# Kernel optimization log

Measured on AMD Instinct MI355X. Metric: run time of the kernel, lower is better.

## Reference

```python
import jax, jax.numpy as jnp
import numpy as np

N_NODES = 50000
BN_EPS = 1e-5


def setup_inputs() -> dict:
    key = jax.random.key(0)
    ks = jax.random.split(key, 10)
    n, e, d, L = N_NODES, 500000, 128, 2
    x = jax.random.normal(ks[0], (n, d), dtype=jnp.float32)
    edge_index = jax.random.randint(ks[1], (2, e), 0, n, dtype=jnp.int64)
    edge_attr = jax.random.normal(ks[2], (e, d), dtype=jnp.float32)
    W1 = jax.random.normal(ks[3], (L, d, d), dtype=jnp.float32) * 0.05
    b1 = jax.random.normal(ks[4], (L, d), dtype=jnp.float32) * 0.02
    gamma = 1.0 + 0.1 * jax.random.normal(ks[5], (L, d), dtype=jnp.float32)
    beta = 0.1 * jax.random.normal(ks[6], (L, d), dtype=jnp.float32)
    W2 = jax.random.normal(ks[7], (L, d, d), dtype=jnp.float32) * 0.05
    b2 = jax.random.normal(ks[8], (L, d), dtype=jnp.float32) * 0.02
    return {"x": x, "edge_index": edge_index, "edge_attr": edge_attr,
            "W1": W1, "b1": b1, "gamma": gamma, "beta": beta, "W2": W2, "b2": b2}


def _gine_layer(x, src, dst, edge_attr, W1l, b1l, gl, bl, W2l, b2l):
    # GINEConv message: relu(x_j + edge_attr), sum-aggregated to target nodes
    msg = jax.nn.relu(x[src] + edge_attr)              # [E, d]
    agg = jax.ops.segment_sum(msg, dst, num_segments=N_NODES)  # [N, d]
    h = (x + agg) @ W1l + b1l                           # eps=0 -> (1+eps)*x = x
    # BatchNorm1d over nodes (train-mode batch stats, biased var)
    mu = jnp.mean(h, axis=0)
    var = jnp.mean(jnp.square(h - mu), axis=0)
    h = (h - mu) * jax.lax.rsqrt(var + BN_EPS) * gl + bl
    h = jax.nn.relu(h)
    h = jax.nn.relu(h @ W2l + b2l)
    return jax.nn.relu(h)  # encoder's outer activation


def reference(x, edge_index, edge_attr, W1, b1, gamma, beta, W2, b2):
    src, dst = edge_index[0], edge_index[1]
    L = W1.shape[0]
    for l in range(L):
        x = _gine_layer(x, src, dst, edge_attr, W1[l], b1[l], gamma[l], beta[l], W2[l], b2[l])
    return x
```

## Files before the change

### kernel.cpp

```cpp
#include <hip/hip_runtime.h>

#define BN_EPS 1e-5f

using f4 = __attribute__((ext_vector_type(4))) float;
using h4 = __attribute__((ext_vector_type(4))) _Float16;

__device__ inline f4 relu4(f4 v) {
    v.x = fmaxf(v.x, 0.f); v.y = fmaxf(v.y, 0.f);
    v.z = fmaxf(v.z, 0.f); v.w = fmaxf(v.w, 0.f);
    return v;
}

__global__ __launch_bounds__(256) void detect_i64_kernel(const int* __restrict__ ei,
                                                         int* __restrict__ flag, int npairs,
                                                         int* __restrict__ deg, int N) {
    __shared__ int ok;
    if (threadIdx.x == 0) ok = 1;
    __syncthreads();
    bool bad = false;
    for (int i = threadIdx.x; i < npairs; i += 256)
        bad |= (ei[2 * i + 1] != 0);
    if (bad) ok = 0;
    int nq = N >> 2;
    int4* d4 = (int4*)deg;
    for (int i = threadIdx.x; i < nq; i += 256) d4[i] = make_int4(0, 0, 0, 0);
    for (int i = (nq << 2) + threadIdx.x; i < N; i += 256) deg[i] = 0;
    __syncthreads();
    if (threadIdx.x == 0) *flag = ok;
}

__global__ __launch_bounds__(256) void canon_kernel(const int* __restrict__ ei,
                                                    const int* __restrict__ flag,
                                                    int* __restrict__ canon,
                                                    int* __restrict__ deg, int n2, int E) {
    int i = blockIdx.x * 256 + threadIdx.x;
    if (i >= n2) return;
    int wide = *flag;
    int v = wide ? ei[2 * i] : ei[i];
    canon[i] = v;
    if (i >= E) atomicAdd(&deg[v], 1);
}

__global__ __launch_bounds__(256) void scan_blk_kernel(const int* __restrict__ deg,
                                                       int* __restrict__ rowptr,
                                                       int* __restrict__ partials, int N) {
    __shared__ int s[256];
    int b = blockIdx.x, t = threadIdx.x;
    int base = b * 1024 + t * 4;
    int4 v = make_int4(0, 0, 0, 0);
    if (base + 3 < N) v = *(const int4*)(deg + base);
    else {
        if (base < N) v.x = deg[base];
        if (base + 1 < N) v.y = deg[base + 1];
        if (base + 2 < N) v.z = deg[base + 2];
        if (base + 3 < N) v.w = deg[base + 3];
    }
    s[t] = v.x + v.y + v.z + v.w;
    __syncthreads();
    for (int off = 1; off < 256; off <<= 1) {
        int u = (t >= off) ? s[t - off] : 0;
        __syncthreads();
        s[t] += u;
        __syncthreads();
    }
    int excl = (t == 0) ? 0 : s[t - 1];
    int4 w;
    w.x = excl;
    w.y = excl + v.x;
    w.z = w.y + v.y;
    w.w = w.z + v.z;
    if (base + 3 < N) *(int4*)(rowptr + base) = w;
    else {
        if (base < N) rowptr[base] = w.x;
        if (base + 1 < N) rowptr[base + 1] = w.y;
        if (base + 2 < N) rowptr[base + 2] = w.z;
        if (base + 3 < N) rowptr[base + 3] = w.w;
    }
    if (t == 255) partials[b] = s[255];
}

__global__ __launch_bounds__(256) void scan_part_kernel(int* __restrict__ partials, int nb) {
    __shared__ int s[256];
    int t = threadIdx.x;
    if (nb <= 256) {
        s[t] = (t < nb) ? partials[t] : 0;
        __syncthreads();
        for (int off = 1; off < 256; off <<= 1) {
            int u = (t >= off) ? s[t - off] : 0;
            __syncthreads();
            s[t] += u;
            __syncthreads();
        }
        if (t < nb) partials[t] = (t == 0) ? 0 : s[t - 1];
    } else if (t == 0) {
        int run = 0;
        for (int i = 0; i < nb; ++i) { int d = partials[i]; partials[i] = run; run += d; }
    }
}

__global__ __launch_bounds__(256) void scan_add_kernel(int* __restrict__ rowptr,
                                                       int* __restrict__ cursor,
                                                       const int* __restrict__ partials,
                                                       float* __restrict__ sums, int nsum,
                                                       int N, int E) {
    int i = blockIdx.x * 256 + threadIdx.x;
    if (i < nsum) sums[i] = 0.f;
    if (i < N) {
        int v = rowptr[i] + partials[i >> 10];
        rowptr[i] = v;
        cursor[i] = v;
    }
    if (i == N) rowptr[N] = E;
}

__global__ __launch_bounds__(256) void fill_kernel(const int* __restrict__ src,
                                                   const int* __restrict__ dst,
                                                   int* __restrict__ cursor,
                                                   int2* __restrict__ pbuf, int E) {
    int e = blockIdx.x * 256 + threadIdx.x;
    if (e >= E) return;
    int d = dst[e];
    int pos = atomicAdd(&cursor[d], 1);
    pbuf[pos] = make_int2(e, src[e]);
}

template <int MODE>
__global__ __launch_bounds__(256) void gather_kernel(const float* __restrict__ x,
                                                     const float* __restrict__ ea,
                                                     _Float16* __restrict__ eah,
                                                     const int* __restrict__ rowptr,
                                                     const int2* __restrict__ pbuf,
                                                     float* __restrict__ aggx, int N) {
    int t = blockIdx.x * 256 + threadIdx.x;
    int n = t >> 5;
    if (n >= N) return;
    int f = t & 31;
    int lo = rowptr[n], hi = rowptr[n + 1];
    f4 acc0 = ((const f4*)(x + (size_t)n * 128))[f];
    f4 acc1 = {0.f, 0.f, 0.f, 0.f};
    f4 acc2 = {0.f, 0.f, 0.f, 0.f};
    f4 acc3 = {0.f, 0.f, 0.f, 0.f};
    int i = lo;
    if (MODE == 1) {
        const h4* ep = (const h4*)eah;
        for (; i + 4 <= hi; i += 4) {
            int2 q0 = pbuf[i];
            int2 q1 = pbuf[i + 1];
            int2 q2 = pbuf[i + 2];
            int2 q3 = pbuf[i + 3];
            f4 xa = ((const f4*)(x + (size_t)q0.y * 128))[f];
            h4 ha = ep[(size_t)i * 32 + f];
            f4 xb = ((const f4*)(x + (size_t)q1.y * 128))[f];
            h4 hb = ep[(size_t)(i + 1) * 32 + f];
            f4 xc = ((const f4*)(x + (size_t)q2.y * 128))[f];
            h4 hc = ep[(size_t)(i + 2) * 32 + f];
            f4 xd = ((const f4*)(x + (size_t)q3.y * 128))[f];
            h4 hd = ep[(size_t)(i + 3) * 32 + f];
            acc0 += relu4(xa + __builtin_convertvector(ha, f4));
            acc1 += relu4(xb + __builtin_convertvector(hb, f4));
            acc2 += relu4(xc + __builtin_convertvector(hc, f4));
            acc3 += relu4(xd + __builtin_convertvector(hd, f4));
        }
        for (; i < hi; ++i) {
            int2 q0 = pbuf[i];
            f4 xa = ((const f4*)(x + (size_t)q0.y * 128))[f];
            h4 ha = ep[(size_t)i * 32 + f];
            acc0 += relu4(xa + __builtin_convertvector(ha, f4));
        }
    } else {
        h4* ep = (h4*)eah;
        for (; i + 4 <= hi; i += 4) {
            int2 q0 = pbuf[i];
            int2 q1 = pbuf[i + 1];
            int2 q2 = pbuf[i + 2];
            int2 q3 = pbuf[i + 3];
            f4 xa = ((const f4*)(x + (size_t)q0.y * 128))[f];
            f4 aa = __builtin_nontemporal_load(((const f4*)(ea + (size_t)q0.x * 128)) + f);
            f4 xb = ((const f4*)(x + (size_t)q1.y * 128))[f];
            f4 ab = __builtin_nontemporal_load(((const f4*)(ea + (size_t)q1.x * 128)) + f);
            f4 xc = ((const f4*)(x + (size_t)q2.y * 128))[f];
            f4 ac = __builtin_nontemporal_load(((const f4*)(ea + (size_t)q2.x * 128)) + f);
            f4 xd = ((const f4*)(x + (size_t)q3.y * 128))[f];
            f4 ad = __builtin_nontemporal_load(((const f4*)(ea + (size_t)q3.x * 128)) + f);
            if (MODE == 0) {
                ep[(size_t)i * 32 + f] = __builtin_convertvector(aa, h4);
                ep[(size_t)(i + 1) * 32 + f] = __builtin_convertvector(ab, h4);
                ep[(size_t)(i + 2) * 32 + f] = __builtin_convertvector(ac, h4);
                ep[(size_t)(i + 3) * 32 + f] = __builtin_convertvector(ad, h4);
            }
            acc0 += relu4(xa + aa);
            acc1 += relu4(xb + ab);
            acc2 += relu4(xc + ac);
            acc3 += relu4(xd + ad);
        }
        for (; i < hi; ++i) {
            int2 q0 = pbuf[i];
            f4 xa = ((const f4*)(x + (size_t)q0.y * 128))[f];
            f4 aa = __builtin_nontemporal_load(((const f4*)(ea + (size_t)q0.x * 128)) + f);
            if (MODE == 0) ep[(size_t)i * 32 + f] = __builtin_convertvector(aa, h4);
            acc0 += relu4(xa + aa);
        }
    }
    f4 r = (acc0 + acc1) + (acc2 + acc3);
    ((f4*)(aggx + (size_t)n * 128))[f] = r;
}

__global__ __launch_bounds__(256) void gemm1_kernel(const float* A,
                                                    const float* __restrict__ W,
                                                    const float* __restrict__ bias,
                                                    float* __restrict__ sums,
                                                    float* out, int N) {
    __shared__ float sA[64][132];
    __shared__ float sW[32][128];
    int t = threadIdx.x;
    int rbase = blockIdx.x * 64;

    {
        int colq = t & 31;
        int r0 = t >> 5;
#pragma unroll
        for (int it = 0; it < 8; ++it) {
            int r = r0 + it * 8;
            int row = rbase + r;
            float4 v = make_float4(0.f, 0.f, 0.f, 0.f);
            if (row < N) v = reinterpret_cast<const float4*>(A + (size_t)row * 128)[colq];
            *reinterpret_cast<float4*>(&sA[r][colq * 4]) = v;
        }
    }

    float acc[4][8];
#pragma unroll
    for (int r = 0; r < 4; ++r)
#pragma unroll
        for (int c = 0; c < 8; ++c) acc[r][c] = 0.f;

    int cg = t & 15, rg = t >> 4;
    int c0a = cg * 4;
    int c0b = 64 + cg * 4;

    for (int kc = 0; kc < 4; ++kc) {
        __syncthreads();
#pragma unroll
        for (int pass = 0; pass < 4; ++pass) {
            int kk = (t >> 5) + pass * 8;
            int k = kc * 32 + kk;
            float4 w = reinterpret_cast<const float4*>(W + (size_t)k * 128)[t & 31];
            *reinterpret_cast<float4*>(&sW[kk][(t & 31) * 4]) = w;
        }
        __syncthreads();
#pragma unroll
        for (int kk0 = 0; kk0 < 32; kk0 += 4) {
            float4 a[4];
#pragma unroll
            for (int r = 0; r < 4; ++r)
                a[r] = *reinterpret_cast<const float4*>(&sA[rg * 4 + r][kc * 32 + kk0]);
#pragma unroll
            for (int j = 0; j < 4; ++j) {
                float4 w0 = *reinterpret_cast<const float4*>(&sW[kk0 + j][c0a]);
                float4 w1 = *reinterpret_cast<const float4*>(&sW[kk0 + j][c0b]);
#pragma unroll
                for (int r = 0; r < 4; ++r) {
                    float av = (j == 0) ? a[r].x : (j == 1) ? a[r].y : (j == 2) ? a[r].z : a[r].w;
                    acc[r][0] += av * w0.x;
                    acc[r][1] += av * w0.y;
                    acc[r][2] += av * w0.z;
                    acc[r][3] += av * w0.w;
                    acc[r][4] += av * w1.x;
                    acc[r][5] += av * w1.y;
                    acc[r][6] += av * w1.z;
                    acc[r][7] += av * w1.w;
                }
            }
        }
    }

    float4 b0 = *reinterpret_cast<const float4*>(bias + c0a);
    float4 b1v = *reinterpret_cast<const float4*>(bias + c0b);
    float cs[8], cs2[8];
#pragma unroll
    for (int j = 0; j < 8; ++j) { cs[j] = 0.f; cs2[j] = 0.f; }

#pragma unroll
    for (int r = 0; r < 4; ++r) {
        int row = rbase + rg * 4 + r;
        if (row >= N) continue;
        float4 o0, o1;
        o0.x = acc[r][0] + b0.x;  o0.y = acc[r][1] + b0.y;
        o0.z = acc[r][2] + b0.z;  o0.w = acc[r][3] + b0.w;
        o1.x = acc[r][4] + b1v.x; o1.y = acc[r][5] + b1v.y;
        o1.z = acc[r][6] + b1v.z; o1.w = acc[r][7] + b1v.w;
        cs[0] += o0.x; cs2[0] += o0.x * o0.x;
        cs[1] += o0.y; cs2[1] += o0.y * o0.y;
        cs[2] += o0.z; cs2[2] += o0.z * o0.z;
        cs[3] += o0.w; cs2[3] += o0.w * o0.w;
        cs[4] += o1.x; cs2[4] += o1.x * o1.x;
        cs[5] += o1.y; cs2[5] += o1.y * o1.y;
        cs[6] += o1.z; cs2[6] += o1.z * o1.z;
        cs[7] += o1.w; cs2[7] += o1.w * o1.w;
        *reinterpret_cast<float4*>(out + (size_t)row * 128 + c0a) = o0;
        *reinterpret_cast<float4*>(out + (size_t)row * 128 + c0b) = o1;
    }

    __syncthreads();
    float* red = &sA[0][0];
    float* red2 = red + 2048;
    int base = (rg * 16 + cg) * 8;
#pragma unroll
    for (int j = 0; j < 8; ++j) { red[base + j] = cs[j]; red2[base + j] = cs2[j]; }
    __syncthreads();
    if (t < 128) {
        int cgj = (t & 63) >> 2;
        int j = (t & 3) + ((t >> 6) << 2);
        float s = 0.f, s2 = 0.f;
#pragma unroll
        for (int rr = 0; rr < 16; ++rr) {
            s += red[(rr * 16 + cgj) * 8 + j];
            s2 += red2[(rr * 16 + cgj) * 8 + j];
        }
        unsafeAtomicAdd(&sums[t], s);
        unsafeAtomicAdd(&sums[128 + t], s2);
    }
}

__global__ __launch_bounds__(256) void gemm2_kernel(const float* __restrict__ A,
                                                    const float* __restrict__ W,
                                                    const float* __restrict__ bias,
                                                    const float* __restrict__ sums,
                                                    const float* __restrict__ gamma,
                                                    const float* __restrict__ beta,
                                                    float* __restrict__ out, int N,
                                                    float invN) {
    __shared__ float sA[64][132];
    __shared__ float sW[32][128];
    __shared__ float sScale[128];
    __shared__ float sShift[128];
    int t = threadIdx.x;
    int rbase = blockIdx.x * 64;

    if (t < 128) {
        float mean = sums[t] * invN;
        float var = sums[128 + t] * invN - mean * mean;
        float inv = rsqrtf(var + BN_EPS);
        float sc = gamma[t] * inv;
        sScale[t] = sc;
        sShift[t] = beta[t] - mean * sc;
    }
    __syncthreads();

    {
        int colq = t & 31;
        int r0 = t >> 5;
        float4 s4 = reinterpret_cast<const float4*>(sScale)[colq];
        float4 sh4 = reinterpret_cast<const float4*>(sShift)[colq];
#pragma unroll
        for (int it = 0; it < 8; ++it) {
            int r = r0 + it * 8;
            int row = rbase + r;
            float4 v = make_float4(0.f, 0.f, 0.f, 0.f);
            if (row < N) {
                float4 a = reinterpret_cast<const float4*>(A + (size_t)row * 128)[colq];
                v.x = fmaxf(a.x * s4.x + sh4.x, 0.f);
                v.y = fmaxf(a.y * s4.y + sh4.y, 0.f);
                v.z = fmaxf(a.z * s4.z + sh4.z, 0.f);
                v.w = fmaxf(a.w * s4.w + sh4.w, 0.f);
            }
            *reinterpret_cast<float4*>(&sA[r][colq * 4]) = v;
        }
    }

    float acc[4][8];
#pragma unroll
    for (int r = 0; r < 4; ++r)
#pragma unroll
        for (int c = 0; c < 8; ++c) acc[r][c] = 0.f;

    int cg = t & 15, rg = t >> 4;
    int c0a = cg * 4;
    int c0b = 64 + cg * 4;

    for (int kc = 0; kc < 4; ++kc) {
        __syncthreads();
#pragma unroll
        for (int pass = 0; pass < 4; ++pass) {
            int kk = (t >> 5) + pass * 8;
            int k = kc * 32 + kk;
            float4 w = reinterpret_cast<const float4*>(W + (size_t)k * 128)[t & 31];
            *reinterpret_cast<float4*>(&sW[kk][(t & 31) * 4]) = w;
        }
        __syncthreads();
#pragma unroll
        for (int kk0 = 0; kk0 < 32; kk0 += 4) {
            float4 a[4];
#pragma unroll
            for (int r = 0; r < 4; ++r)
                a[r] = *reinterpret_cast<const float4*>(&sA[rg * 4 + r][kc * 32 + kk0]);
#pragma unroll
            for (int j = 0; j < 4; ++j) {
                float4 w0 = *reinterpret_cast<const float4*>(&sW[kk0 + j][c0a]);
                float4 w1 = *reinterpret_cast<const float4*>(&sW[kk0 + j][c0b]);
#pragma unroll
                for (int r = 0; r < 4; ++r) {
                    float av = (j == 0) ? a[r].x : (j == 1) ? a[r].y : (j == 2) ? a[r].z : a[r].w;
                    acc[r][0] += av * w0.x;
                    acc[r][1] += av * w0.y;
                    acc[r][2] += av * w0.z;
                    acc[r][3] += av * w0.w;
                    acc[r][4] += av * w1.x;
                    acc[r][5] += av * w1.y;
                    acc[r][6] += av * w1.z;
                    acc[r][7] += av * w1.w;
                }
            }
        }
    }

    float4 b0 = *reinterpret_cast<const float4*>(bias + c0a);
    float4 b1v = *reinterpret_cast<const float4*>(bias + c0b);
#pragma unroll
    for (int r = 0; r < 4; ++r) {
        int row = rbase + rg * 4 + r;
        if (row >= N) continue;
        float4 o0, o1;
        o0.x = fmaxf(acc[r][0] + b0.x, 0.f);  o0.y = fmaxf(acc[r][1] + b0.y, 0.f);
        o0.z = fmaxf(acc[r][2] + b0.z, 0.f);  o0.w = fmaxf(acc[r][3] + b0.w, 0.f);
        o1.x = fmaxf(acc[r][4] + b1v.x, 0.f); o1.y = fmaxf(acc[r][5] + b1v.y, 0.f);
        o1.z = fmaxf(acc[r][6] + b1v.z, 0.f); o1.w = fmaxf(acc[r][7] + b1v.w, 0.f);
        *reinterpret_cast<float4*>(out + (size_t)row * 128 + c0a) = o0;
        *reinterpret_cast<float4*>(out + (size_t)row * 128 + c0b) = o1;
    }
}

extern "C" void kernel_launch(void* const* d_in, const int* in_sizes, int n_in,
                              void* d_out, int out_size, void* d_ws, size_t ws_size,
                              hipStream_t stream) {
    const float* x     = (const float*)d_in[0];
    const int*   ei    = (const int*)d_in[1];
    const float* ea    = (const float*)d_in[2];
    const float* W1    = (const float*)d_in[3];
    const float* b1    = (const float*)d_in[4];
    const float* gamma = (const float*)d_in[5];
    const float* beta  = (const float*)d_in[6];
    const float* W2    = (const float*)d_in[7];
    const float* b2    = (const float*)d_in[8];

    int N = in_sizes[0] / 128;
    int E = in_sizes[2] / 128;
    int L = in_sizes[3] / (128 * 128);

    size_t NF = (size_t)N * 128;
    float*     buf    = (float*)d_ws;
    float*     sums   = buf + NF;
    _Float16*  eah    = (_Float16*)(sums + 256 * L);
    int*       canon  = (int*)(eah + (size_t)E * 128);
    int*       deg    = canon + (size_t)2 * E;
    int*       rowptr = deg + N;
    int*       cursor = rowptr + N + 2;
    int2*      pbuf   = (int2*)(cursor + N);
    int*       partials = (int*)(pbuf + E);
    int*       flag   = partials + ((N + 1023) / 1024) + 1;

    int npairs = (E < 4096) ? E : 4096;
    detect_i64_kernel<<<1, 256, 0, stream>>>(ei, flag, npairs, deg, N);
    int E2 = 2 * E;
    canon_kernel<<<(E2 + 255) / 256, 256, 0, stream>>>(ei, flag, canon, deg, E2, E);
    const int* src = canon;
    const int* dst = canon + E;

    int nb = (N + 1023) / 1024;
    scan_blk_kernel<<<nb, 256, 0, stream>>>(deg, rowptr, partials, N);
    scan_part_kernel<<<1, 256, 0, stream>>>(partials, nb);
    scan_add_kernel<<<(N + 256) / 256, 256, 0, stream>>>(rowptr, cursor, partials,
                                                         sums, 256 * L, N, E);
    int eBlocks = (E + 255) / 256;
    fill_kernel<<<eBlocks, 256, 0, stream>>>(src, dst, cursor, pbuf, E);

    int gatherBlocks = (N * 32 + 255) / 256;
    int gemmBlocks = (N + 63) / 64;
    float invN = 1.0f / (float)N;
    const float* xin = x;
    for (int l = 0; l < L; ++l) {
        float* xout = (float*)d_out;
        float* sums_l = sums + (size_t)l * 256;
        if (l == 0) {
            if (L > 1)
                gather_kernel<0><<<gatherBlocks, 256, 0, stream>>>(xin, ea, eah, rowptr,
                                                                   pbuf, buf, N);
            else
                gather_kernel<2><<<gatherBlocks, 256, 0, stream>>>(xin, ea, eah, rowptr,
                                                                   pbuf, buf, N);
        } else {
            gather_kernel<1><<<gatherBlocks, 256, 0, stream>>>(xin, ea, eah, rowptr,
                                                               pbuf, buf, N);
        }
        gemm1_kernel<<<gemmBlocks, 256, 0, stream>>>(buf, W1 + (size_t)l * 16384,
                                                     b1 + (size_t)l * 128, sums_l, buf, N);
        gemm2_kernel<<<gemmBlocks, 256, 0, stream>>>(buf, W2 + (size_t)l * 16384,
                                                     b2 + (size_t)l * 128, sums_l,
                                                     gamma + (size_t)l * 128,
                                                     beta + (size_t)l * 128, xout, N, invN);
        xin = xout;
    }
}
```

Before: 673.3 us.

## Store node features in fp16 for neighbor gathers

Adds a cast kernel that converts the input node features to fp16 in the output buffer. The layer-0 gemm2 now writes its activations as fp16 directly into that buffer, and the gather kernels read neighbor rows as fp16 and convert them to fp32 before accumulating. This halves the bytes moved by the random per-edge x gathers, at the cost of an extra cast pass and reduced precision in the aggregation. The final layer still writes fp32 output.

```diff
diff --git a/kernel.cpp b/kernel.cpp
--- a/kernel.cpp
+++ b/kernel.cpp
@@ -124,8 +124,16 @@
     pbuf[pos] = make_int2(e, src[e]);
 }
 
+__global__ __launch_bounds__(256) void castx_kernel(const float* __restrict__ x,
+                                                    _Float16* __restrict__ x16, int nq) {
+    int i = blockIdx.x * 256 + threadIdx.x;
+    if (i >= nq) return;
+    f4 v = ((const f4*)x)[i];
+    ((h4*)x16)[i] = __builtin_convertvector(v, h4);
+}
+
 template <int MODE>
-__global__ __launch_bounds__(256) void gather_kernel(const float* __restrict__ x,
+__global__ __launch_bounds__(256) void gather_kernel(const _Float16* __restrict__ x16,
                                                      const float* __restrict__ ea,
                                                      _Float16* __restrict__ eah,
                                                      const int* __restrict__ rowptr,
@@ -136,7 +144,8 @@
     if (n >= N) return;
     int f = t & 31;
     int lo = rowptr[n], hi = rowptr[n + 1];
-    f4 acc0 = ((const f4*)(x + (size_t)n * 128))[f];
+    const h4* xp = (const h4*)x16;
+    f4 acc0 = __builtin_convertvector(xp[(size_t)n * 32 + f], f4);
     f4 acc1 = {0.f, 0.f, 0.f, 0.f};
     f4 acc2 = {0.f, 0.f, 0.f, 0.f};
     f4 acc3 = {0.f, 0.f, 0.f, 0.f};
@@ -148,24 +157,24 @@
             int2 q1 = pbuf[i + 1];
             int2 q2 = pbuf[i + 2];
             int2 q3 = pbuf[i + 3];
-            f4 xa = ((const f4*)(x + (size_t)q0.y * 128))[f];
+            h4 xa = xp[(size_t)q0.y * 32 + f];
             h4 ha = ep[(size_t)i * 32 + f];
-            f4 xb = ((const f4*)(x + (size_t)q1.y * 128))[f];
+            h4 xb = xp[(size_t)q1.y * 32 + f];
             h4 hb = ep[(size_t)(i + 1) * 32 + f];
-            f4 xc = ((const f4*)(x + (size_t)q2.y * 128))[f];
+            h4 xc = xp[(size_t)q2.y * 32 + f];
             h4 hc = ep[(size_t)(i + 2) * 32 + f];
-            f4 xd = ((const f4*)(x + (size_t)q3.y * 128))[f];
+            h4 xd = xp[(size_t)q3.y * 32 + f];
             h4 hd = ep[(size_t)(i + 3) * 32 + f];
-            acc0 += relu4(xa + __builtin_convertvector(ha, f4));
-            acc1 += relu4(xb + __builtin_convertvector(hb, f4));
-            acc2 += relu4(xc + __builtin_convertvector(hc, f4));
-            acc3 += relu4(xd + __builtin_convertvector(hd, f4));
+            acc0 += relu4(__builtin_convertvector(xa, f4) + __builtin_convertvector(ha, f4));
+            acc1 += relu4(__builtin_convertvector(xb, f4) + __builtin_convertvector(hb, f4));
+            acc2 += relu4(__builtin_convertvector(xc, f4) + __builtin_convertvector(hc, f4));
+            acc3 += relu4(__builtin_convertvector(xd, f4) + __builtin_convertvector(hd, f4));
         }
         for (; i < hi; ++i) {
             int2 q0 = pbuf[i];
-            f4 xa = ((const f4*)(x + (size_t)q0.y * 128))[f];
+            h4 xa = xp[(size_t)q0.y * 32 + f];
             h4 ha = ep[(size_t)i * 32 + f];
-            acc0 += relu4(xa + __builtin_convertvector(ha, f4));
+            acc0 += relu4(__builtin_convertvector(xa, f4) + __builtin_convertvector(ha, f4));
         }
     } else {
         h4* ep = (h4*)eah;
@@ -174,13 +183,13 @@
             int2 q1 = pbuf[i + 1];
             int2 q2 = pbuf[i + 2];
             int2 q3 = pbuf[i + 3];
-            f4 xa = ((const f4*)(x + (size_t)q0.y * 128))[f];
+            h4 xa = xp[(size_t)q0.y * 32 + f];
             f4 aa = __builtin_nontemporal_load(((const f4*)(ea + (size_t)q0.x * 128)) + f);
-            f4 xb = ((const f4*)(x + (size_t)q1.y * 128))[f];
+            h4 xb = xp[(size_t)q1.y * 32 + f];
             f4 ab = __builtin_nontemporal_load(((const f4*)(ea + (size_t)q1.x * 128)) + f);
-            f4 xc = ((const f4*)(x + (size_t)q2.y * 128))[f];
+            h4 xc = xp[(size_t)q2.y * 32 + f];
             f4 ac = __builtin_nontemporal_load(((const f4*)(ea + (size_t)q2.x * 128)) + f);
-            f4 xd = ((const f4*)(x + (size_t)q3.y * 128))[f];
+            h4 xd = xp[(size_t)q3.y * 32 + f];
             f4 ad = __builtin_nontemporal_load(((const f4*)(ea + (size_t)q3.x * 128)) + f);
             if (MODE == 0) {
                 ep[(size_t)i * 32 + f] = __builtin_convertvector(aa, h4);
@@ -188,17 +197,17 @@
                 ep[(size_t)(i + 2) * 32 + f] = __builtin_convertvector(ac, h4);
                 ep[(size_t)(i + 3) * 32 + f] = __builtin_convertvector(ad, h4);
             }
-            acc0 += relu4(xa + aa);
-            acc1 += relu4(xb + ab);
-            acc2 += relu4(xc + ac);
-            acc3 += relu4(xd + ad);
+            acc0 += relu4(__builtin_convertvector(xa, f4) + aa);
+            acc1 += relu4(__builtin_convertvector(xb, f4) + ab);
+            acc2 += relu4(__builtin_convertvector(xc, f4) + ac);
+            acc3 += relu4(__builtin_convertvector(xd, f4) + ad);
         }
         for (; i < hi; ++i) {
             int2 q0 = pbuf[i];
-            f4 xa = ((const f4*)(x + (size_t)q0.y * 128))[f];
+            h4 xa = xp[(size_t)q0.y * 32 + f];
             f4 aa = __builtin_nontemporal_load(((const f4*)(ea + (size_t)q0.x * 128)) + f);
             if (MODE == 0) ep[(size_t)i * 32 + f] = __builtin_convertvector(aa, h4);
-            acc0 += relu4(xa + aa);
+            acc0 += relu4(__builtin_convertvector(xa, f4) + aa);
         }
     }
     f4 r = (acc0 + acc1) + (acc2 + acc3);
@@ -322,13 +331,15 @@
     }
 }
 
+template <int WX16>
 __global__ __launch_bounds__(256) void gemm2_kernel(const float* __restrict__ A,
                                                     const float* __restrict__ W,
                                                     const float* __restrict__ bias,
                                                     const float* __restrict__ sums,
                                                     const float* __restrict__ gamma,
                                                     const float* __restrict__ beta,
-                                                    float* __restrict__ out, int N,
+                                                    float* __restrict__ out,
+                                                    _Float16* __restrict__ x16, int N,
                                                     float invN) {
     __shared__ float sA[64][132];
     __shared__ float sW[32][128];
@@ -420,13 +431,19 @@
     for (int r = 0; r < 4; ++r) {
         int row = rbase + rg * 4 + r;
         if (row >= N) continue;
-        float4 o0, o1;
+        f4 o0, o1;
         o0.x = fmaxf(acc[r][0] + b0.x, 0.f);  o0.y = fmaxf(acc[r][1] + b0.y, 0.f);
         o0.z = fmaxf(acc[r][2] + b0.z, 0.f);  o0.w = fmaxf(acc[r][3] + b0.w, 0.f);
         o1.x = fmaxf(acc[r][4] + b1v.x, 0.f); o1.y = fmaxf(acc[r][5] + b1v.y, 0.f);
         o1.z = fmaxf(acc[r][6] + b1v.z, 0.f); o1.w = fmaxf(acc[r][7] + b1v.w, 0.f);
-        *reinterpret_cast<float4*>(out + (size_t)row * 128 + c0a) = o0;
-        *reinterpret_cast<float4*>(out + (size_t)row * 128 + c0b) = o1;
+        if (WX16) {
+            h4* xp = (h4*)(x16 + (size_t)row * 128);
+            xp[cg] = __builtin_convertvector(o0, h4);
+            xp[16 + cg] = __builtin_convertvector(o1, h4);
+        } else {
+            *reinterpret_cast<f4*>(out + (size_t)row * 128 + c0a) = o0;
+            *reinterpret_cast<f4*>(out + (size_t)row * 128 + c0b) = o1;
+        }
     }
 }
 
@@ -459,6 +476,8 @@
     int*       partials = (int*)(pbuf + E);
     int*       flag   = partials + ((N + 1023) / 1024) + 1;
 
+    _Float16* x16 = (_Float16*)d_out;
+
     int npairs = (E < 4096) ? E : 4096;
     detect_i64_kernel<<<1, 256, 0, stream>>>(ei, flag, npairs, deg, N);
     int E2 = 2 * E;
@@ -473,31 +492,38 @@
                                                          sums, 256 * L, N, E);
     int eBlocks = (E + 255) / 256;
     fill_kernel<<<eBlocks, 256, 0, stream>>>(src, dst, cursor, pbuf, E);
+    int nq = (int)(NF >> 2);
+    castx_kernel<<<(nq + 255) / 256, 256, 0, stream>>>(x, x16, nq);
 
     int gatherBlocks = (N * 32 + 255) / 256;
     int gemmBlocks = (N + 63) / 64;
     float invN = 1.0f / (float)N;
-    const float* xin = x;
     for (int l = 0; l < L; ++l) {
-        float* xout = (float*)d_out;
         float* sums_l = sums + (size_t)l * 256;
         if (l == 0) {
             if (L > 1)
-                gather_kernel<0><<<gatherBlocks, 256, 0, stream>>>(xin, ea, eah, rowptr,
+                gather_kernel<0><<<gatherBlocks, 256, 0, stream>>>(x16, ea, eah, rowptr,
                                                                    pbuf, buf, N);
             else
-                gather_kernel<2><<<gatherBlocks, 256, 0, stream>>>(xin, ea, eah, rowptr,
+                gather_kernel<2><<<gatherBlocks, 256, 0, stream>>>(x16, ea, eah, rowptr,
                                                                    pbuf, buf, N);
         } else {
-            gather_kernel<1><<<gatherBlocks, 256, 0, stream>>>(xin, ea, eah, rowptr,
+            gather_kernel<1><<<gatherBlocks, 256, 0, stream>>>(x16, ea, eah, rowptr,
                                                                pbuf, buf, N);
         }
         gemm1_kernel<<<gemmBlocks, 256, 0, stream>>>(buf, W1 + (size_t)l * 16384,
                                                      b1 + (size_t)l * 128, sums_l, buf, N);
-        gemm2_kernel<<<gemmBlocks, 256, 0, stream>>>(buf, W2 + (size_t)l * 16384,
-                                                     b2 + (size_t)l * 128, sums_l,
-                                                     gamma + (size_t)l * 128,
-                                                     beta + (size_t)l * 128, xout, N, invN);
-        xin = xout;
-    }
-}
+        if (l < L - 1)
+            gemm2_kernel<1><<<gemmBlocks, 256, 0, stream>>>(buf, W2 + (size_t)l * 16384,
+                                                            b2 + (size_t)l * 128, sums_l,
+                                                            gamma + (size_t)l * 128,
+                                                            beta + (size_t)l * 128,
+                                                            (float*)d_out, x16, N, invN);
+        else
+            gemm2_kernel<0><<<gemmBlocks, 256, 0, stream>>>(buf, W2 + (size_t)l * 16384,
+                                                            b2 + (size_t)l * 128, sums_l,
+                                                            gamma + (size_t)l * 128,
+                                                            beta + (size_t)l * 128,
+                                                            (float*)d_out, x16, N, invN);
+    }
+}
```

Measured after the change: 654.8 us. 2.8% less time.
